# Performance work log

Hardware: AMD Instinct MI355X
Metric: run time of the kernel (lower is better)

Reference implementation:

```python
import jax, jax.numpy as jnp
import numpy as np

ALPHA = 0.1  # init kwarg alpha


def setup_inputs() -> dict:
    key = jax.random.key(0)
    k1, k2 = jax.random.split(key)
    x = jax.random.normal(k1, (32, 192, 64, 64), dtype=jnp.float32)
    delta = jax.random.normal(k2, (32, 1, 64, 64), dtype=jnp.float32)
    return {"x_bchw": x, "delta": delta}


def reference(x_bchw, delta):
    # Faithful fixed-shape version of LayerTokenPrune.forward.
    # Kept tokens are stream-compacted to the front (stable, preserving
    # original token order, matching torch.where index order); dropped
    # positions are zero-padded, matching the zero-pad in the original.
    B, C, H, W = x_bchw.shape
    L = H * W
    tok = jnp.transpose(x_bchw, (0, 2, 3, 1)).reshape(B, L, C)  # [B, L, C]

    delta_tok = delta.reshape(B, -1)  # 4-dim delta branch -> [B, L]
    imp = jnp.abs(delta_tok)
    lo = imp.min(axis=1, keepdims=True)
    hi = imp.max(axis=1, keepdims=True)
    rng = jnp.maximum(hi - lo, 1e-3)  # clamp_min(0.001)
    imp = (imp - lo) / rng

    mu = imp.mean(axis=1, keepdims=True)
    sigma = imp.std(axis=1, keepdims=True, ddof=1)  # torch std is unbiased
    theta = mu - ALPHA * sigma
    keep = imp >= theta  # [B, L] bool; max-imp token always kept (theta<=mu<=1)

    # Stable compaction: kept token indices first, in original order.
    # jnp.argsort is stable, so sorting the key (0 for keep, 1 for drop)
    # reproduces torch.where's ascending-index order for kept tokens.
    order = jnp.argsort(jnp.logical_not(keep).astype(jnp.int32), axis=1)  # [B, L]
    gathered = jnp.take_along_axis(tok, order[:, :, None], axis=1)  # [B, L, C]

    counts = keep.sum(axis=1)  # [B]
    valid = (jnp.arange(L)[None, :] < counts[:, None]).astype(tok.dtype)  # [B, L]
    tok_new = gathered * valid[:, :, None]  # zero out pad positions

    # Fixed-shape analogue of the sqrt reshape: pad to full L = H*W grid.
    y = tok_new.reshape(B, H, W, C).transpose(0, 3, 1, 2)  # [B, C, H, W]

    keep_ratio = counts.astype(jnp.float32).mean() / L
    theta_mean = theta.mean()
    return y, keep_ratio, theta_mean
```

## Files before the change

kernel.cpp:

```cpp
#include <hip/hip_runtime.h>
#include <hip/hip_bf16.h>
#include <math.h>

#define B_ 32
#define C_ 192
#define H_ 64
#define W_ 64
#define L_ 4096
#define L4_ 1024
#define NTHREADS 256
#define PER_THREAD 16

typedef float  f32x4 __attribute__((ext_vector_type(4)));

__global__ __launch_bounds__(NTHREADS) void stats_scan_kernel(
    const float* __restrict__ delta,
    int*  __restrict__ src_idx,
    int*  __restrict__ counts,
    float* __restrict__ thetas)
{
  const int b = blockIdx.x;
  const int t = threadIdx.x;
  const int lane = t & 63;
  const int wid  = t >> 6;

  __shared__ float  smin[4], smax[4];
  __shared__ float  s_lo, s_rng, s_theta;
  __shared__ double dsum[4], dsum2[4];
  __shared__ int    wsum[4];

  const float* dp = delta + (size_t)b * L_;

  float a[PER_THREAD];
  const float4* d4 = (const float4*)dp;
  #pragma unroll
  for (int i = 0; i < 4; ++i) {
    float4 v = d4[t * 4 + i];
    a[i*4+0] = fabsf(v.x); a[i*4+1] = fabsf(v.y);
    a[i*4+2] = fabsf(v.z); a[i*4+3] = fabsf(v.w);
  }

  float lmin = a[0], lmax = a[0];
  #pragma unroll
  for (int i = 1; i < PER_THREAD; ++i) {
    lmin = fminf(lmin, a[i]);
    lmax = fmaxf(lmax, a[i]);
  }
  #pragma unroll
  for (int off = 32; off; off >>= 1) {
    lmin = fminf(lmin, __shfl_down(lmin, off, 64));
    lmax = fmaxf(lmax, __shfl_down(lmax, off, 64));
  }
  if (lane == 0) { smin[wid] = lmin; smax[wid] = lmax; }
  __syncthreads();
  if (t == 0) {
    float lo = fminf(fminf(smin[0], smin[1]), fminf(smin[2], smin[3]));
    float hi = fmaxf(fmaxf(smax[0], smax[1]), fmaxf(smax[2], smax[3]));
    s_lo  = lo;
    s_rng = fmaxf(hi - lo, 1e-3f);
  }
  __syncthreads();
  const float lo  = s_lo;
  const float rng = s_rng;

  double s = 0.0, s2 = 0.0;
  #pragma unroll
  for (int i = 0; i < PER_THREAD; ++i) {
    float imp = (a[i] - lo) / rng;
    a[i] = imp;
    s  += (double)imp;
    s2 += (double)imp * (double)imp;
  }
  #pragma unroll
  for (int off = 32; off; off >>= 1) {
    s  += __shfl_down(s,  off, 64);
    s2 += __shfl_down(s2, off, 64);
  }
  if (lane == 0) { dsum[wid] = s; dsum2[wid] = s2; }
  __syncthreads();
  if (t == 0) {
    double S  = dsum[0]  + dsum[1]  + dsum[2]  + dsum[3];
    double S2 = dsum2[0] + dsum2[1] + dsum2[2] + dsum2[3];
    double mu  = S / (double)L_;
    double var = (S2 - S * S / (double)L_) / (double)(L_ - 1);
    if (var < 0.0) var = 0.0;
    double sigma = sqrt(var);
    s_theta = (float)(mu - 0.1 * sigma);
  }
  __syncthreads();
  const float theta = s_theta;

  int flags = 0, cnt = 0;
  #pragma unroll
  for (int i = 0; i < PER_THREAD; ++i) {
    int k = (a[i] >= theta) ? 1 : 0;
    cnt += k;
    flags |= (k << i);
  }
  int inc = cnt;
  #pragma unroll
  for (int off = 1; off < 64; off <<= 1) {
    int y = __shfl_up(inc, off, 64);
    if (lane >= off) inc += y;
  }
  if (lane == 63) wsum[wid] = inc;
  __syncthreads();
  int base = inc - cnt;
  #pragma unroll
  for (int w = 0; w < 4; ++w)
    if (w < wid) base += wsum[w];

  int* sb = src_idx + (size_t)b * L_;
  int p = base;
  #pragma unroll
  for (int i = 0; i < PER_THREAD; ++i) {
    if ((flags >> i) & 1) { sb[p++] = t * PER_THREAD + i; }
  }
  if (t == NTHREADS - 1) {
    counts[b] = base + cnt;
    thetas[b] = theta;
  }
}

__global__ __launch_bounds__(64) void finalize_kernel(
    const int* __restrict__ counts, const float* __restrict__ thetas,
    float* __restrict__ out_tail)
{
  const int t = threadIdx.x;
  float c  = (t < B_) ? (float)counts[t] : 0.0f;
  float th = (t < B_) ? thetas[t]        : 0.0f;
  #pragma unroll
  for (int off = 32; off; off >>= 1) {
    c  += __shfl_down(c,  off, 64);
    th += __shfl_down(th, off, 64);
  }
  if (t == 0) {
    out_tail[0] = (c / (float)B_) / (float)L_;
    out_tail[1] = th / (float)B_;
  }
}

__global__ __launch_bounds__(NTHREADS) void gather_kernel(
    const float* __restrict__ x,
    const int*  __restrict__ src_idx,
    const int*  __restrict__ counts,
    float* __restrict__ out)
{
  __shared__ float row[L_];

  const int bc = blockIdx.x;
  const int b  = bc / C_;
  const int t  = threadIdx.x;

  const float4* x4 = (const float4*)(x + (size_t)bc * L_);
  float4* r4 = (float4*)row;

  #pragma unroll
  for (int i = 0; i < 4; ++i) {
    r4[t + NTHREADS * i] = x4[t + NTHREADS * i];
  }
  __syncthreads();

  const int  cnt = counts[b];
  const int4* s4b = (const int4*)(src_idx + (size_t)b * L_);
  f32x4* o4 = (f32x4*)(out + (size_t)bc * L_);

  #pragma unroll
  for (int i = 0; i < 4; ++i) {
    const int j  = t + NTHREADS * i;
    const int d0 = j * 4;
    const int4 s = s4b[j];
    f32x4 r;
    r.x = (d0 + 0 < cnt) ? row[s.x] : 0.0f;
    r.y = (d0 + 1 < cnt) ? row[s.y] : 0.0f;
    r.z = (d0 + 2 < cnt) ? row[s.z] : 0.0f;
    r.w = (d0 + 3 < cnt) ? row[s.w] : 0.0f;
    __builtin_nontemporal_store(r, o4 + j);
  }
}

extern "C" void kernel_launch(void* const* d_in, const int* in_sizes, int n_in,
                              void* d_out, int out_size, void* d_ws, size_t ws_size,
                              hipStream_t stream) {
  const float* x     = (const float*)d_in[0];
  const float* delta = (const float*)d_in[1];
  float* out = (float*)d_out;

  int*   src_idx = (int*)d_ws;
  int*   counts  = (int*)((char*)d_ws + (size_t)B_ * L_ * 4);
  float* thetas  = (float*)((char*)d_ws + (size_t)B_ * L_ * 4 + 128);

  const size_t y_elems = (size_t)B_ * C_ * L_;

  stats_scan_kernel<<<B_, NTHREADS, 0, stream>>>(delta, src_idx, counts, thetas);
  finalize_kernel<<<1, 64, 0, stream>>>(counts, thetas, out + y_elems);
  gather_kernel<<<B_ * C_, NTHREADS, 0, stream>>>(x, src_idx, counts, out);
}
```

Measured before the change: 185.4 us.

## Process 8 channels per block with double-buffered LDS and fuse finalize

The gather kernel now handles 8 channels per block instead of one. It loads the compaction indices once per block and double-buffers each channel's row in shared memory, with the next row's global load issued while the current row is gathered. The separate finalize kernel is folded into block 0 of the gather kernel, which removes one launch. The trade-offs are a 32KB LDS footprint, fewer blocks in flight, and more registers per thread.

Result: slower. 191.5 us (+3.3%).

```diff
diff --git a/kernel.cpp b/kernel.cpp
--- a/kernel.cpp
+++ b/kernel.cpp
@@ -1,5 +1,4 @@
 #include <hip/hip_runtime.h>
-#include <hip/hip_bf16.h>
 #include <math.h>
 
 #define B_ 32
@@ -10,6 +9,8 @@
 #define L4_ 1024
 #define NTHREADS 256
 #define PER_THREAD 16
+#define CPB 8
+#define CG_ (C_ / CPB)
 
 typedef float  f32x4 __attribute__((ext_vector_type(4)));
 
@@ -122,60 +123,84 @@
   }
 }
 
-__global__ __launch_bounds__(64) void finalize_kernel(
-    const int* __restrict__ counts, const float* __restrict__ thetas,
-    float* __restrict__ out_tail)
-{
-  const int t = threadIdx.x;
-  float c  = (t < B_) ? (float)counts[t] : 0.0f;
-  float th = (t < B_) ? thetas[t]        : 0.0f;
-  #pragma unroll
-  for (int off = 32; off; off >>= 1) {
-    c  += __shfl_down(c,  off, 64);
-    th += __shfl_down(th, off, 64);
-  }
-  if (t == 0) {
-    out_tail[0] = (c / (float)B_) / (float)L_;
-    out_tail[1] = th / (float)B_;
-  }
-}
-
 __global__ __launch_bounds__(NTHREADS) void gather_kernel(
     const float* __restrict__ x,
     const int*  __restrict__ src_idx,
     const int*  __restrict__ counts,
-    float* __restrict__ out)
+    const float* __restrict__ thetas,
+    float* __restrict__ out,
+    float* __restrict__ out_tail)
 {
-  __shared__ float row[L_];
-
-  const int bc = blockIdx.x;
-  const int b  = bc / C_;
-  const int t  = threadIdx.x;
-
-  const float4* x4 = (const float4*)(x + (size_t)bc * L_);
-  float4* r4 = (float4*)row;
-
-  #pragma unroll
-  for (int i = 0; i < 4; ++i) {
-    r4[t + NTHREADS * i] = x4[t + NTHREADS * i];
-  }
-  __syncthreads();
-
-  const int  cnt = counts[b];
+  __shared__ float buf[2][L_];
+
+  const int blk = blockIdx.x;
+  const int b   = blk / CG_;
+  const int cg  = blk % CG_;
+  const int t   = threadIdx.x;
+
+  if (blk == 0 && t < 64) {
+    float c  = (t < B_) ? (float)counts[t] : 0.0f;
+    float th = (t < B_) ? thetas[t]        : 0.0f;
+    #pragma unroll
+    for (int off = 32; off; off >>= 1) {
+      c  += __shfl_down(c,  off, 64);
+      th += __shfl_down(th, off, 64);
+    }
+    if (t == 0) {
+      out_tail[0] = (c / (float)B_) / (float)L_;
+      out_tail[1] = th / (float)B_;
+    }
+  }
+
+  const size_t rowbase = ((size_t)b * C_ + (size_t)cg * CPB) * L_;
+  const float4* x4 = (const float4*)(x + rowbase);
+  f32x4*        o4 = (f32x4*)(out + rowbase);
+
+  const int cnt = counts[b];
+  int4 s[4];
   const int4* s4b = (const int4*)(src_idx + (size_t)b * L_);
-  f32x4* o4 = (f32x4*)(out + (size_t)bc * L_);
-
-  #pragma unroll
-  for (int i = 0; i < 4; ++i) {
-    const int j  = t + NTHREADS * i;
-    const int d0 = j * 4;
-    const int4 s = s4b[j];
-    f32x4 r;
-    r.x = (d0 + 0 < cnt) ? row[s.x] : 0.0f;
-    r.y = (d0 + 1 < cnt) ? row[s.y] : 0.0f;
-    r.z = (d0 + 2 < cnt) ? row[s.z] : 0.0f;
-    r.w = (d0 + 3 < cnt) ? row[s.w] : 0.0f;
-    __builtin_nontemporal_store(r, o4 + j);
+  #pragma unroll
+  for (int i = 0; i < 4; ++i) s[i] = s4b[t + NTHREADS * i];
+
+  float4 st[4];
+  #pragma unroll
+  for (int i = 0; i < 4; ++i) st[i] = x4[t + NTHREADS * i];
+  {
+    float4* w = (float4*)buf[0];
+    #pragma unroll
+    for (int i = 0; i < 4; ++i) w[t + NTHREADS * i] = st[i];
+  }
+  __syncthreads();
+
+  #pragma unroll
+  for (int k = 0; k < CPB; ++k) {
+    if (k + 1 < CPB) {
+      const float4* xn = x4 + (size_t)(k + 1) * L4_;
+      #pragma unroll
+      for (int i = 0; i < 4; ++i) st[i] = xn[t + NTHREADS * i];
+    }
+
+    const float* cur = buf[k & 1];
+    f32x4* ok = o4 + (size_t)k * L4_;
+    #pragma unroll
+    for (int i = 0; i < 4; ++i) {
+      const int j  = t + NTHREADS * i;
+      const int d0 = j * 4;
+      const int4 si = s[i];
+      f32x4 r;
+      r.x = (d0 + 0 < cnt) ? cur[si.x & (L_ - 1)] : 0.0f;
+      r.y = (d0 + 1 < cnt) ? cur[si.y & (L_ - 1)] : 0.0f;
+      r.z = (d0 + 2 < cnt) ? cur[si.z & (L_ - 1)] : 0.0f;
+      r.w = (d0 + 3 < cnt) ? cur[si.w & (L_ - 1)] : 0.0f;
+      __builtin_nontemporal_store(r, ok + j);
+    }
+
+    if (k + 1 < CPB) {
+      float4* w = (float4*)buf[(k + 1) & 1];
+      #pragma unroll
+      for (int i = 0; i < 4; ++i) w[t + NTHREADS * i] = st[i];
+    }
+    __syncthreads();
   }
 }
 
@@ -193,6 +218,6 @@
   const size_t y_elems = (size_t)B_ * C_ * L_;
 
   stats_scan_kernel<<<B_, NTHREADS, 0, stream>>>(delta, src_idx, counts, thetas);
-  finalize_kernel<<<1, 64, 0, stream>>>(counts, thetas, out + y_elems);
-  gather_kernel<<<B_ * C_, NTHREADS, 0, stream>>>(x, src_idx, counts, out);
+  gather_kernel<<<B_ * CG_, NTHREADS, 0, stream>>>(x, src_idx, counts, thetas,
+                                                   out, out + y_elems);
 }
```

## Split gather into three channel-slab launches with mixed LDS-load and store paths

Applied to the files above, without the earlier changes.

Removes the separate finalize kernel and folds it into the first gather launch. The gather is split into three launches over channel slabs of 64. Each launch uses a different strategy: direct global-to-LDS loads with nontemporal stores, direct LDS loads with normal stores, or the original register-staged load with normal stores. Gather indices are masked to stay in range. This saves one launch but adds two more. It looks like an experiment that mixes load and store paths, with the risk of extra launch overhead and uneven cache behavior.

After: 191.6 us. +3.3%, slower.

```diff
diff --git a/kernel.cpp b/kernel.cpp
--- a/kernel.cpp
+++ b/kernel.cpp
@@ -1,5 +1,4 @@
 #include <hip/hip_runtime.h>
-#include <hip/hip_bf16.h>
 #include <math.h>
 
 #define B_ 32
@@ -10,6 +9,7 @@
 #define L4_ 1024
 #define NTHREADS 256
 #define PER_THREAD 16
+#define CSPLIT 64
 
 typedef float  f32x4 __attribute__((ext_vector_type(4)));
 
@@ -122,48 +122,63 @@
   }
 }
 
-__global__ __launch_bounds__(64) void finalize_kernel(
-    const int* __restrict__ counts, const float* __restrict__ thetas,
-    float* __restrict__ out_tail)
-{
-  const int t = threadIdx.x;
-  float c  = (t < B_) ? (float)counts[t] : 0.0f;
-  float th = (t < B_) ? thetas[t]        : 0.0f;
-  #pragma unroll
-  for (int off = 32; off; off >>= 1) {
-    c  += __shfl_down(c,  off, 64);
-    th += __shfl_down(th, off, 64);
-  }
-  if (t == 0) {
-    out_tail[0] = (c / (float)B_) / (float)L_;
-    out_tail[1] = th / (float)B_;
-  }
-}
-
+template <int MODE>
 __global__ __launch_bounds__(NTHREADS) void gather_kernel(
     const float* __restrict__ x,
     const int*  __restrict__ src_idx,
     const int*  __restrict__ counts,
-    float* __restrict__ out)
+    const float* __restrict__ thetas,
+    float* __restrict__ out,
+    float* __restrict__ out_tail,
+    int c0)
 {
   __shared__ float row[L_];
 
-  const int bc = blockIdx.x;
-  const int b  = bc / C_;
-  const int t  = threadIdx.x;
-
-  const float4* x4 = (const float4*)(x + (size_t)bc * L_);
-  float4* r4 = (float4*)row;
-
-  #pragma unroll
-  for (int i = 0; i < 4; ++i) {
-    r4[t + NTHREADS * i] = x4[t + NTHREADS * i];
+  const int blk = blockIdx.x;
+  const int b   = blk / CSPLIT;
+  const int c   = c0 + (blk % CSPLIT);
+  const int t   = threadIdx.x;
+
+  if (MODE == 0 && blk == 0 && t < 64) {
+    float cc = (t < B_) ? (float)counts[t] : 0.0f;
+    float th = (t < B_) ? thetas[t]        : 0.0f;
+    #pragma unroll
+    for (int off = 32; off; off >>= 1) {
+      cc += __shfl_down(cc, off, 64);
+      th += __shfl_down(th, off, 64);
+    }
+    if (t == 0) {
+      out_tail[0] = (cc / (float)B_) / (float)L_;
+      out_tail[1] = th / (float)B_;
+    }
+  }
+
+  const size_t rowbase = ((size_t)b * C_ + (size_t)c) * L_;
+  const float* xr = x + rowbase;
+
+  if (MODE == 2) {
+    const float4* x4 = (const float4*)xr;
+    float4* r4 = (float4*)row;
+    #pragma unroll
+    for (int i = 0; i < 4; ++i) r4[t + NTHREADS * i] = x4[t + NTHREADS * i];
+  } else {
+    const int lane = t & 63;
+    const int w    = t >> 6;
+    #pragma unroll
+    for (int k = 0; k < 4; ++k) {
+      const int seg = w * 4 + k;
+      const float* gp = xr + ((size_t)seg * 64 + lane) * 4;
+      __builtin_amdgcn_global_load_lds(
+          (const __attribute__((address_space(1))) void*)gp,
+          (__attribute__((address_space(3))) void*)((char*)row + seg * 1024),
+          16, 0, 0);
+    }
   }
   __syncthreads();
 
   const int  cnt = counts[b];
   const int4* s4b = (const int4*)(src_idx + (size_t)b * L_);
-  f32x4* o4 = (f32x4*)(out + (size_t)bc * L_);
+  f32x4* o4 = (f32x4*)(out + rowbase);
 
   #pragma unroll
   for (int i = 0; i < 4; ++i) {
@@ -171,11 +186,15 @@
     const int d0 = j * 4;
     const int4 s = s4b[j];
     f32x4 r;
-    r.x = (d0 + 0 < cnt) ? row[s.x] : 0.0f;
-    r.y = (d0 + 1 < cnt) ? row[s.y] : 0.0f;
-    r.z = (d0 + 2 < cnt) ? row[s.z] : 0.0f;
-    r.w = (d0 + 3 < cnt) ? row[s.w] : 0.0f;
-    __builtin_nontemporal_store(r, o4 + j);
+    r.x = (d0 + 0 < cnt) ? row[s.x & (L_ - 1)] : 0.0f;
+    r.y = (d0 + 1 < cnt) ? row[s.y & (L_ - 1)] : 0.0f;
+    r.z = (d0 + 2 < cnt) ? row[s.z & (L_ - 1)] : 0.0f;
+    r.w = (d0 + 3 < cnt) ? row[s.w & (L_ - 1)] : 0.0f;
+    if (MODE == 0) {
+      __builtin_nontemporal_store(r, o4 + j);
+    } else {
+      o4[j] = r;
+    }
   }
 }
 
@@ -191,8 +210,15 @@
   float* thetas  = (float*)((char*)d_ws + (size_t)B_ * L_ * 4 + 128);
 
   const size_t y_elems = (size_t)B_ * C_ * L_;
+  float* out_tail = out + y_elems;
 
   stats_scan_kernel<<<B_, NTHREADS, 0, stream>>>(delta, src_idx, counts, thetas);
-  finalize_kernel<<<1, 64, 0, stream>>>(counts, thetas, out + y_elems);
-  gather_kernel<<<B_ * C_, NTHREADS, 0, stream>>>(x, src_idx, counts, out);
+
+  const int grid = B_ * CSPLIT;
+  gather_kernel<0><<<grid, NTHREADS, 0, stream>>>(x, src_idx, counts, thetas,
+                                                  out, out_tail, 0);
+  gather_kernel<1><<<grid, NTHREADS, 0, stream>>>(x, src_idx, counts, thetas,
+                                                  out, out_tail, CSPLIT);
+  gather_kernel<2><<<grid, NTHREADS, 0, stream>>>(x, src_idx, counts, thetas,
+                                                  out, out_tail, 2 * CSPLIT);
 }
```

## Gather directly from global memory and fold finalize into gather kernel

Applied to the files above, without the earlier changes.

Removes the LDS staging of each 16KB input row: the gather now reads the x values straight from global memory, relying on cache since the kept indices are mostly ascending. It also skips the index load and reads for pad positions past the kept count, drops the nontemporal store hint, and merges the tiny finalize kernel into block 0 of the gather kernel, which saves one launch. The risk is scattered uncoalesced global loads instead of LDS reads, and regular stores that may pollute cache.

Measured after the change: 190.7 us. 2.8% more time.

```diff
diff --git a/kernel.cpp b/kernel.cpp
--- a/kernel.cpp
+++ b/kernel.cpp
@@ -1,5 +1,4 @@
 #include <hip/hip_runtime.h>
-#include <hip/hip_bf16.h>
 #include <math.h>
 
 #define B_ 32
@@ -122,60 +121,51 @@
   }
 }
 
-__global__ __launch_bounds__(64) void finalize_kernel(
-    const int* __restrict__ counts, const float* __restrict__ thetas,
-    float* __restrict__ out_tail)
-{
-  const int t = threadIdx.x;
-  float c  = (t < B_) ? (float)counts[t] : 0.0f;
-  float th = (t < B_) ? thetas[t]        : 0.0f;
-  #pragma unroll
-  for (int off = 32; off; off >>= 1) {
-    c  += __shfl_down(c,  off, 64);
-    th += __shfl_down(th, off, 64);
-  }
-  if (t == 0) {
-    out_tail[0] = (c / (float)B_) / (float)L_;
-    out_tail[1] = th / (float)B_;
-  }
-}
-
 __global__ __launch_bounds__(NTHREADS) void gather_kernel(
     const float* __restrict__ x,
     const int*  __restrict__ src_idx,
     const int*  __restrict__ counts,
-    float* __restrict__ out)
+    const float* __restrict__ thetas,
+    float* __restrict__ out,
+    float* __restrict__ out_tail)
 {
-  __shared__ float row[L_];
-
   const int bc = blockIdx.x;
   const int b  = bc / C_;
   const int t  = threadIdx.x;
 
-  const float4* x4 = (const float4*)(x + (size_t)bc * L_);
-  float4* r4 = (float4*)row;
+  if (bc == 0 && t < 64) {
+    float cc = (t < B_) ? (float)counts[t] : 0.0f;
+    float th = (t < B_) ? thetas[t]        : 0.0f;
+    #pragma unroll
+    for (int off = 32; off; off >>= 1) {
+      cc += __shfl_down(cc, off, 64);
+      th += __shfl_down(th, off, 64);
+    }
+    if (t == 0) {
+      out_tail[0] = (cc / (float)B_) / (float)L_;
+      out_tail[1] = th / (float)B_;
+    }
+  }
 
-  #pragma unroll
-  for (int i = 0; i < 4; ++i) {
-    r4[t + NTHREADS * i] = x4[t + NTHREADS * i];
-  }
-  __syncthreads();
-
-  const int  cnt = counts[b];
-  const int4* s4b = (const int4*)(src_idx + (size_t)b * L_);
-  f32x4* o4 = (f32x4*)(out + (size_t)bc * L_);
+  const size_t rowbase = (size_t)bc * L_;
+  const float* xr  = x + rowbase;
+  const int    cnt = counts[b];
+  const int4*  s4b = (const int4*)(src_idx + (size_t)b * L_);
+  f32x4*       o4  = (f32x4*)(out + rowbase);
 
   #pragma unroll
   for (int i = 0; i < 4; ++i) {
     const int j  = t + NTHREADS * i;
     const int d0 = j * 4;
-    const int4 s = s4b[j];
-    f32x4 r;
-    r.x = (d0 + 0 < cnt) ? row[s.x] : 0.0f;
-    r.y = (d0 + 1 < cnt) ? row[s.y] : 0.0f;
-    r.z = (d0 + 2 < cnt) ? row[s.z] : 0.0f;
-    r.w = (d0 + 3 < cnt) ? row[s.w] : 0.0f;
-    __builtin_nontemporal_store(r, o4 + j);
+    f32x4 r = {0.0f, 0.0f, 0.0f, 0.0f};
+    if (d0 < cnt) {
+      const int4 s = s4b[j];
+      r.x = xr[s.x & (L_ - 1)];
+      r.y = (d0 + 1 < cnt) ? xr[s.y & (L_ - 1)] : 0.0f;
+      r.z = (d0 + 2 < cnt) ? xr[s.z & (L_ - 1)] : 0.0f;
+      r.w = (d0 + 3 < cnt) ? xr[s.w & (L_ - 1)] : 0.0f;
+    }
+    o4[j] = r;
   }
 }
 
@@ -191,8 +181,9 @@
   float* thetas  = (float*)((char*)d_ws + (size_t)B_ * L_ * 4 + 128);
 
   const size_t y_elems = (size_t)B_ * C_ * L_;
+  float* out_tail = out + y_elems;
 
   stats_scan_kernel<<<B_, NTHREADS, 0, stream>>>(delta, src_idx, counts, thetas);
-  finalize_kernel<<<1, 64, 0, stream>>>(counts, thetas, out + y_elems);
-  gather_kernel<<<B_ * C_, NTHREADS, 0, stream>>>(x, src_idx, counts, out);
+  gather_kernel<<<B_ * C_, NTHREADS, 0, stream>>>(x, src_idx, counts, thetas,
+                                                  out, out_tail);
 }
```
